# Performance work log

Hardware: AMD Instinct MI355X
Metric: run time of the kernel (lower is better)

The kernel has to match this reference:

```python
import jax, jax.numpy as jnp
import numpy as np

EPS = 1e-16
LOG_2PI = float(np.log(2.0 * np.pi))
DUMMY = -2.0 * float(np.log(10.0))  # dummy component logit / log-prob


def setup_inputs() -> dict:
    key = jax.random.key(0)
    k1, k2, k3, k4, k5 = jax.random.split(key, 5)
    B, N, V, D = 32, 1024, 512, 4
    x = jax.random.normal(k1, (B, N, D), dtype=jnp.float32)
    votes = jax.random.normal(k2, (B, V, D), dtype=jnp.float32)
    # positive stds in [0.1, 1.0)
    scales = jax.random.uniform(k3, (B, V), dtype=jnp.float32) * 0.9 + 0.1
    vote_presence_prob = jax.random.uniform(k4, (B, V), dtype=jnp.float32)
    presence = jax.random.uniform(k5, (B, N), dtype=jnp.float32)
    return {"x": x, "votes": votes, "scales": scales,
            "vote_presence_prob": vote_presence_prob,
            "presence": presence, "n_votes": 16}


def reference(x, votes, scales, vote_presence_prob, presence, n_votes):
    B, N, D = x.shape
    V = votes.shape[1]
    # Broadcast Normal log-prob: x [B,N,1,D] vs votes [B,1,V,D], scale [B,1,V,1]
    sig = scales[:, None, :, None]
    z = (x[:, :, None, :] - votes[:, None, :, :]) / sig
    lp_per_dim = -0.5 * z * z - jnp.log(sig) - 0.5 * LOG_2PI
    vote_log_prob = jnp.sum(lp_per_dim, axis=-1)                       # [B,N,V]
    vote_log_prob = jnp.concatenate(
        [vote_log_prob, jnp.full((B, N, 1), DUMMY, vote_log_prob.dtype)], axis=2)  # [B,N,V+1]

    mixing_logits = jnp.log(vote_presence_prob + EPS)                  # safe_log, [B,V]
    mixing_logits = jnp.concatenate(
        [mixing_logits, jnp.full((B, 1), DUMMY, mixing_logits.dtype)], axis=1)     # [B,V+1]
    mixing_log_prob = jax.nn.log_softmax(mixing_logits, axis=1)        # [B,V+1]

    posterior = mixing_log_prob[:, None, :] + vote_log_prob            # [B,N,V+1]
    mixture_lp_per_comp = jax.scipy.special.logsumexp(posterior, axis=2)  # [B,N]
    mixture_lp_per_comp = mixture_lp_per_comp * presence
    log_prob = jnp.sum(mixture_lp_per_comp)                            # scalar

    winning_vote_idx = jnp.argmax(posterior[:, :, :-1], axis=2)        # [B,N]
    winner = jnp.take_along_axis(votes, winning_vote_idx[:, :, None], axis=1)  # [B,N,D]
    winner_pres = jnp.take_along_axis(vote_presence_prob, winning_vote_idx, axis=1)  # [B,N]
    vote_presence = (mixing_logits[:, :-1] > mixing_logits[:, -1:]).astype(jnp.float32)  # [B,V]
    is_from_capsule = winning_vote_idx // n_votes                      # [B,N]
    posterior_mixing_probs = jax.nn.softmax(posterior, axis=-1)[..., :-1]  # [B,N,V]

    return (log_prob, vote_presence, winner, winner_pres, is_from_capsule,
            mixing_logits, mixing_log_prob, jnp.zeros_like(winner),
            jnp.zeros_like(winner_pres), posterior_mixing_probs)
```

## Files before the change

### kernel.cpp

```cpp
#include <hip/hip_runtime.h>

#define FEPS 1e-16f
#define LOG_2PI 1.8378770664093453f
#define DUMMYV -4.605170185988091f

constexpr int B = 32, N = 1024, V = 512, D = 4;

constexpr long long OFF_LOGPROB    = 0;
constexpr long long OFF_VOTEPRES   = 1;
constexpr long long OFF_WINNER     = OFF_VOTEPRES + (long long)B * V;
constexpr long long OFF_WINNERPRES = OFF_WINNER + (long long)B * N * D;
constexpr long long OFF_ISFROM     = OFF_WINNERPRES + (long long)B * N;
constexpr long long OFF_MLOGITS    = OFF_ISFROM + (long long)B * N;
constexpr long long OFF_MLOGPROB   = OFF_MLOGITS + (long long)B * (V + 1);
constexpr long long OFF_ZW         = OFF_MLOGPROB + (long long)B * (V + 1);
constexpr long long OFF_ZWP        = OFF_ZW + (long long)B * N * D;
constexpr long long OFF_PMP        = OFF_ZWP + (long long)B * N;

__global__ __launch_bounds__(256) void k_fused(const float* __restrict__ x,
                                               const float* __restrict__ votes,
                                               const float* __restrict__ scales,
                                               const float* __restrict__ vpp,
                                               const float* __restrict__ presence,
                                               const int* __restrict__ nv_p,
                                               float* __restrict__ out,
                                               float* __restrict__ ws_partial) {
    __shared__ float4 s_v4[V];
    __shared__ float s_h[V], s_cpre[V], s_lg[V], s_vpp[V];
    __shared__ float s_redm[4], s_reds[4], s_part[4];

    int b = blockIdx.y;
    int t = threadIdx.x;
    int w = t >> 6, lane = t & 63;

    float lgv[2];
    #pragma unroll
    for (int i = 0; i < 2; ++i) {
        int v = t + i * 256;
        float4 vt = reinterpret_cast<const float4*>(votes)[(long long)b * V + v];
        float sv  = scales[(long long)b * V + v];
        float pp  = vpp[(long long)b * V + v];
        float lg  = logf(pp + FEPS);
        float inv = 1.0f / sv;
        s_v4[v]   = vt;
        s_vpp[v]  = pp;
        s_lg[v]   = lg;
        s_h[v]    = 0.5f * inv * inv;
        s_cpre[v] = lg - 4.0f * logf(sv) - 2.0f * LOG_2PI;
        lgv[i] = lg;
    }
    __syncthreads();

    float m = fmaxf(lgv[0], lgv[1]);
    #pragma unroll
    for (int o = 32; o > 0; o >>= 1) m = fmaxf(m, __shfl_xor(m, o));
    if (lane == 0) s_redm[w] = m;
    __syncthreads();
    float M = fmaxf(fmaxf(fmaxf(s_redm[0], s_redm[1]), fmaxf(s_redm[2], s_redm[3])), DUMMYV);
    float s = expf(lgv[0] - M) + expf(lgv[1] - M);
    #pragma unroll
    for (int o = 32; o > 0; o >>= 1) s += __shfl_xor(s, o);
    if (lane == 0) s_reds[w] = s;
    __syncthreads();
    float S = s_reds[0] + s_reds[1] + s_reds[2] + s_reds[3] + expf(DUMMYV - M);
    float lse = M + logf(S);

    float hk[8], c2k[8], hvx[8], hvy[8], hvz[8], hvw[8];
    #pragma unroll
    for (int k = 0; k < 8; ++k) {
        int v = k * 64 + lane;
        float4 vv = s_v4[v];
        float h = s_h[v];
        float c = s_cpre[v] - lse;
        float v2 = vv.x * vv.x + vv.y * vv.y + vv.z * vv.z + vv.w * vv.w;
        hk[k]  = h;
        c2k[k] = c - h * v2;
        hvx[k] = 2.0f * h * vv.x;
        hvy[k] = 2.0f * h * vv.y;
        hvz[k] = 2.0f * h * vv.z;
        hvw[k] = 2.0f * h * vv.w;
    }
    float dummy_post = DUMMYV + (DUMMYV - lse);
    int nv = nv_p[0];
    float acc = 0.f;

    #pragma unroll
    for (int iter = 0; iter < 4; ++iter) {
        int n = blockIdx.x * 16 + iter * 4 + w;
        long long bn = (long long)b * N + n;
        float4 xv = reinterpret_cast<const float4*>(x)[bn];
        float nxx2 = -(xv.x * xv.x + xv.y * xv.y + xv.z * xv.z + xv.w * xv.w);

        float p[8];
        float bv = -1e30f;
        int bi = 0;
        #pragma unroll
        for (int k = 0; k < 8; ++k) {
            float pv = fmaf(hk[k], nxx2, c2k[k]);
            pv = fmaf(hvx[k], xv.x, pv);
            pv = fmaf(hvy[k], xv.y, pv);
            pv = fmaf(hvz[k], xv.z, pv);
            pv = fmaf(hvw[k], xv.w, pv);
            p[k] = pv;
            if (pv > bv) { bv = pv; bi = k * 64 + lane; }
        }
        #pragma unroll
        for (int o = 32; o > 0; o >>= 1) {
            float ov = __shfl_xor(bv, o);
            int   oi = __shfl_xor(bi, o);
            if (ov > bv || (ov == bv && oi < bi)) { bv = ov; bi = oi; }
        }

        float M2 = fmaxf(bv, dummy_post);
        float e[8];
        float lsum = 0.f;
        #pragma unroll
        for (int k = 0; k < 8; ++k) { e[k] = __expf(p[k] - M2); lsum += e[k]; }
        #pragma unroll
        for (int o = 32; o > 0; o >>= 1) lsum += __shfl_xor(lsum, o);
        float total = lsum + __expf(dummy_post - M2);
        float rtot  = 1.0f / total;

        long long base = OFF_PMP + bn * V;
        #pragma unroll
        for (int k = 0; k < 8; ++k)
            out[base + k * 64 + lane] = e[k] * rtot;

        if (lane == 0) {
            acc += (M2 + logf(total)) * presence[bn];
            float4 wv = s_v4[bi];
            out[OFF_WINNER + bn * 4 + 0] = wv.x;
            out[OFF_WINNER + bn * 4 + 1] = wv.y;
            out[OFF_WINNER + bn * 4 + 2] = wv.z;
            out[OFF_WINNER + bn * 4 + 3] = wv.w;
            out[OFF_WINNERPRES + bn]     = s_vpp[bi];
            out[OFF_ISFROM + bn]         = (float)(bi / nv);
        }
        if (lane == 1) {
            out[OFF_ZW + bn * 4 + 0] = 0.f;
            out[OFF_ZW + bn * 4 + 1] = 0.f;
            out[OFF_ZW + bn * 4 + 2] = 0.f;
            out[OFF_ZW + bn * 4 + 3] = 0.f;
            out[OFF_ZWP + bn]        = 0.f;
        }
    }

    if (lane == 0) s_part[w] = acc;
    __syncthreads();
    if (t == 0)
        ws_partial[(long long)b * gridDim.x + blockIdx.x] =
            s_part[0] + s_part[1] + s_part[2] + s_part[3];

    if (blockIdx.x == 0) {
        #pragma unroll
        for (int i = 0; i < 2; ++i) {
            int v = t + i * 256;
            float ml = s_lg[v];
            out[OFF_MLOGITS  + (long long)b * (V + 1) + v] = ml;
            out[OFF_MLOGPROB + (long long)b * (V + 1) + v] = ml - lse;
            out[OFF_VOTEPRES + (long long)b * V + v]       = (ml > DUMMYV) ? 1.0f : 0.0f;
        }
        if (t == 0) {
            out[OFF_MLOGITS  + (long long)b * (V + 1) + V] = DUMMYV;
            out[OFF_MLOGPROB + (long long)b * (V + 1) + V] = DUMMYV - lse;
        }
    }
}

__global__ __launch_bounds__(256) void k_reduce(const float* __restrict__ ws_partial,
                                                float* __restrict__ out, int count) {
    __shared__ float sred[256];
    int t = threadIdx.x;
    float s = 0.f;
    for (int i = t; i < count; i += 256) s += ws_partial[i];
    sred[t] = s;
    __syncthreads();
    for (int o = 128; o > 0; o >>= 1) {
        if (t < o) sred[t] += sred[t + o];
        __syncthreads();
    }
    if (t == 0) out[OFF_LOGPROB] = sred[0];
}

extern "C" void kernel_launch(void* const* d_in, const int* in_sizes, int n_in,
                              void* d_out, int out_size, void* d_ws, size_t ws_size,
                              hipStream_t stream) {
    const float* x        = (const float*)d_in[0];
    const float* votes    = (const float*)d_in[1];
    const float* scales   = (const float*)d_in[2];
    const float* vpp      = (const float*)d_in[3];
    const float* presence = (const float*)d_in[4];
    const int*   nv       = (const int*)d_in[5];
    float* out = (float*)d_out;
    float* ws  = (float*)d_ws;

    dim3 g(N / 16, B);
    k_fused<<<g, 256, 0, stream>>>(x, votes, scales, vpp, presence, nv, out, ws);
    k_reduce<<<1, 256, 0, stream>>>(ws, out, (N / 16) * B);
}
```

Before: 31.88 us.

## Rewrite fused mixture kernel with DPP reductions, packed math, and dummy-relative exp2

Each wave now computes its own per-batch coefficients directly from global memory, so the shared-memory staging and block barriers for the vote tables are gone. Logits are pre-shifted by the dummy posterior and scaled by log2(e), so a raw exp2 replaces the per-row max subtraction and the total becomes sum plus one. Argmax becomes a wave max followed by a min-index search. Wave reductions use DPP row rotates, and the inner product uses packed two-wide float vectors. Each block handles twice as many rows, which halves the number of blocks and partial sums and amortises setup, at the risk of exp2 overflow with no max subtraction.

```diff
diff --git a/kernel.cpp b/kernel.cpp
--- a/kernel.cpp
+++ b/kernel.cpp
@@ -1,140 +1,216 @@
 #include <hip/hip_runtime.h>
+
+typedef float v2f __attribute__((ext_vector_type(2)));
 
 #define FEPS 1e-16f
 #define LOG_2PI 1.8378770664093453f
 #define DUMMYV -4.605170185988091f
-
-constexpr int B = 32, N = 1024, V = 512, D = 4;
+#define LOG2E 1.4426950408889634f
+#define LN2 0.6931471805599453f
+
+constexpr int B = 32, N = 1024, V = 512;
 
 constexpr long long OFF_LOGPROB    = 0;
 constexpr long long OFF_VOTEPRES   = 1;
 constexpr long long OFF_WINNER     = OFF_VOTEPRES + (long long)B * V;
-constexpr long long OFF_WINNERPRES = OFF_WINNER + (long long)B * N * D;
+constexpr long long OFF_WINNERPRES = OFF_WINNER + (long long)B * N * 4;
 constexpr long long OFF_ISFROM     = OFF_WINNERPRES + (long long)B * N;
 constexpr long long OFF_MLOGITS    = OFF_ISFROM + (long long)B * N;
 constexpr long long OFF_MLOGPROB   = OFF_MLOGITS + (long long)B * (V + 1);
 constexpr long long OFF_ZW         = OFF_MLOGPROB + (long long)B * (V + 1);
-constexpr long long OFF_ZWP        = OFF_ZW + (long long)B * N * D;
+constexpr long long OFF_ZWP        = OFF_ZW + (long long)B * N * 4;
 constexpr long long OFF_PMP        = OFF_ZWP + (long long)B * N;
+
+__device__ __forceinline__ float fexp2(float x) {
+#if __has_builtin(__builtin_amdgcn_exp2f)
+    return __builtin_amdgcn_exp2f(x);
+#else
+    return __expf(x * LN2);
+#endif
+}
+__device__ __forceinline__ float frcp(float x) {
+#if __has_builtin(__builtin_amdgcn_rcpf)
+    return __builtin_amdgcn_rcpf(x);
+#else
+    return 1.0f / x;
+#endif
+}
+
+template<int RN> __device__ __forceinline__ float dppRorF(float x) {
+    return __int_as_float(__builtin_amdgcn_update_dpp(
+        0, __float_as_int(x), 0x120 | RN, 0xF, 0xF, false));
+}
+template<int RN> __device__ __forceinline__ int dppRorI(int x) {
+    return __builtin_amdgcn_update_dpp(0, x, 0x120 | RN, 0xF, 0xF, false);
+}
+
+__device__ __forceinline__ float waveMaxF(float m) {
+    m = fmaxf(m, dppRorF<1>(m));
+    m = fmaxf(m, dppRorF<2>(m));
+    m = fmaxf(m, dppRorF<4>(m));
+    m = fmaxf(m, dppRorF<8>(m));
+    m = fmaxf(m, __shfl_xor(m, 16));
+    m = fmaxf(m, __shfl_xor(m, 32));
+    return m;
+}
+__device__ __forceinline__ float waveSumF(float s) {
+    s += dppRorF<1>(s);
+    s += dppRorF<2>(s);
+    s += dppRorF<4>(s);
+    s += dppRorF<8>(s);
+    s += __shfl_xor(s, 16);
+    s += __shfl_xor(s, 32);
+    return s;
+}
+__device__ __forceinline__ int waveMinI(int v) {
+    int o;
+    o = dppRorI<1>(v); v = o < v ? o : v;
+    o = dppRorI<2>(v); v = o < v ? o : v;
+    o = dppRorI<4>(v); v = o < v ? o : v;
+    o = dppRorI<8>(v); v = o < v ? o : v;
+    o = __shfl_xor(v, 16); v = o < v ? o : v;
+    o = __shfl_xor(v, 32); v = o < v ? o : v;
+    return v;
+}
 
 __global__ __launch_bounds__(256) void k_fused(const float* __restrict__ x,
                                                const float* __restrict__ votes,
                                                const float* __restrict__ scales,
                                                const float* __restrict__ vpp,
                                                const float* __restrict__ presence,
-                                               const int* __restrict__ nv_p,
+                                               const int* __restrict__ nvp,
                                                float* __restrict__ out,
-                                               float* __restrict__ ws_partial) {
-    __shared__ float4 s_v4[V];
-    __shared__ float s_h[V], s_cpre[V], s_lg[V], s_vpp[V];
-    __shared__ float s_redm[4], s_reds[4], s_part[4];
-
-    int b = blockIdx.y;
-    int t = threadIdx.x;
-    int w = t >> 6, lane = t & 63;
-
-    float lgv[2];
-    #pragma unroll
-    for (int i = 0; i < 2; ++i) {
-        int v = t + i * 256;
-        float4 vt = reinterpret_cast<const float4*>(votes)[(long long)b * V + v];
-        float sv  = scales[(long long)b * V + v];
-        float pp  = vpp[(long long)b * V + v];
-        float lg  = logf(pp + FEPS);
-        float inv = 1.0f / sv;
-        s_v4[v]   = vt;
-        s_vpp[v]  = pp;
-        s_lg[v]   = lg;
-        s_h[v]    = 0.5f * inv * inv;
-        s_cpre[v] = lg - 4.0f * logf(sv) - 2.0f * LOG_2PI;
-        lgv[i] = lg;
-    }
-    __syncthreads();
-
-    float m = fmaxf(lgv[0], lgv[1]);
-    #pragma unroll
-    for (int o = 32; o > 0; o >>= 1) m = fmaxf(m, __shfl_xor(m, o));
-    if (lane == 0) s_redm[w] = m;
-    __syncthreads();
-    float M = fmaxf(fmaxf(fmaxf(s_redm[0], s_redm[1]), fmaxf(s_redm[2], s_redm[3])), DUMMYV);
-    float s = expf(lgv[0] - M) + expf(lgv[1] - M);
-    #pragma unroll
-    for (int o = 32; o > 0; o >>= 1) s += __shfl_xor(s, o);
-    if (lane == 0) s_reds[w] = s;
-    __syncthreads();
-    float S = s_reds[0] + s_reds[1] + s_reds[2] + s_reds[3] + expf(DUMMYV - M);
-    float lse = M + logf(S);
-
-    float hk[8], c2k[8], hvx[8], hvy[8], hvz[8], hvw[8];
+                                               float* __restrict__ ws) {
+    __shared__ float s_part[4];
+    const int b = blockIdx.y, t = threadIdx.x, w = t >> 6, lane = t & 63;
+    const long long bV = (long long)b * V;
+    const float4* votes4 = reinterpret_cast<const float4*>(votes) + bV;
+
+    float lg[8], lsv[8];
+    float4 vt[8];
     #pragma unroll
     for (int k = 0; k < 8; ++k) {
         int v = k * 64 + lane;
-        float4 vv = s_v4[v];
-        float h = s_h[v];
-        float c = s_cpre[v] - lse;
-        float v2 = vv.x * vv.x + vv.y * vv.y + vv.z * vv.z + vv.w * vv.w;
-        hk[k]  = h;
-        c2k[k] = c - h * v2;
-        hvx[k] = 2.0f * h * vv.x;
-        hvy[k] = 2.0f * h * vv.y;
-        hvz[k] = 2.0f * h * vv.z;
-        hvw[k] = 2.0f * h * vv.w;
-    }
+        vt[k]  = votes4[v];
+        lsv[k] = scales[bV + v];
+        lg[k]  = __logf(vpp[bV + v] + FEPS);
+    }
+
+    float mm = lg[0];
+    #pragma unroll
+    for (int k = 1; k < 8; ++k) mm = fmaxf(mm, lg[k]);
+    float M = fmaxf(waveMaxF(mm), DUMMYV);
+    float ss = 0.f;
+    #pragma unroll
+    for (int k = 0; k < 8; ++k) ss += __expf(lg[k] - M);
+    float S = waveSumF(ss) + __expf(DUMMYV - M);
+    float lse = M + __logf(S);
     float dummy_post = DUMMYV + (DUMMYV - lse);
-    int nv = nv_p[0];
+
+    if (blockIdx.x == 0 && w == 0) {
+        #pragma unroll
+        for (int k = 0; k < 8; ++k) {
+            int v = k * 64 + lane;
+            out[OFF_MLOGITS  + (long long)b * (V + 1) + v] = lg[k];
+            out[OFF_MLOGPROB + (long long)b * (V + 1) + v] = lg[k] - lse;
+            out[OFF_VOTEPRES + bV + v] = (lg[k] > DUMMYV) ? 1.0f : 0.0f;
+        }
+        if (lane == 0) {
+            out[OFF_MLOGITS  + (long long)b * (V + 1) + V] = DUMMYV;
+            out[OFF_MLOGPROB + (long long)b * (V + 1) + V] = DUMMYV - lse;
+        }
+    }
+
+    v2f c2[4], hk[4], hvx[4], hvy[4], hvz[4], hvw[4];
+    #pragma unroll
+    for (int i = 0; i < 4; ++i) {
+        float cc[2], kk[2], ax[2], ay[2], az[2], aw[2];
+        #pragma unroll
+        for (int h = 0; h < 2; ++h) {
+            int k = 2 * i + h;
+            float sv  = lsv[k];
+            float inv = frcp(sv);
+            float hh  = 0.5f * inv * inv;
+            float c   = lg[k] - 4.0f * __logf(sv) - 2.0f * LOG_2PI - lse;
+            float4 vv = vt[k];
+            float v2  = vv.x * vv.x + vv.y * vv.y + vv.z * vv.z + vv.w * vv.w;
+            cc[h] = (c - hh * v2 - dummy_post) * LOG2E;
+            kk[h] = -hh * LOG2E;
+            float g = 2.0f * hh * LOG2E;
+            ax[h] = g * vv.x; ay[h] = g * vv.y; az[h] = g * vv.z; aw[h] = g * vv.w;
+        }
+        c2[i].x = cc[0];  c2[i].y = cc[1];
+        hk[i].x = kk[0];  hk[i].y = kk[1];
+        hvx[i].x = ax[0]; hvx[i].y = ax[1];
+        hvy[i].x = ay[0]; hvy[i].y = ay[1];
+        hvz[i].x = az[0]; hvz[i].y = az[1];
+        hvw[i].x = aw[0]; hvw[i].y = aw[1];
+    }
+
+    const float4* x4 = reinterpret_cast<const float4*>(x) + (long long)b * N;
+    const long long pmpB = OFF_PMP + ((long long)b * N) * V;
+    int nv = nvp[0];
     float acc = 0.f;
 
-    #pragma unroll
-    for (int iter = 0; iter < 4; ++iter) {
-        int n = blockIdx.x * 16 + iter * 4 + w;
+    #pragma unroll 2
+    for (int iter = 0; iter < 8; ++iter) {
+        int n = blockIdx.x * 32 + iter * 4 + w;
         long long bn = (long long)b * N + n;
-        float4 xv = reinterpret_cast<const float4*>(x)[bn];
-        float nxx2 = -(xv.x * xv.x + xv.y * xv.y + xv.z * xv.z + xv.w * xv.w);
-
-        float p[8];
-        float bv = -1e30f;
-        int bi = 0;
-        #pragma unroll
-        for (int k = 0; k < 8; ++k) {
-            float pv = fmaf(hk[k], nxx2, c2k[k]);
-            pv = fmaf(hvx[k], xv.x, pv);
-            pv = fmaf(hvy[k], xv.y, pv);
-            pv = fmaf(hvz[k], xv.z, pv);
-            pv = fmaf(hvw[k], xv.w, pv);
-            p[k] = pv;
-            if (pv > bv) { bv = pv; bi = k * 64 + lane; }
-        }
-        #pragma unroll
-        for (int o = 32; o > 0; o >>= 1) {
-            float ov = __shfl_xor(bv, o);
-            int   oi = __shfl_xor(bi, o);
-            if (ov > bv || (ov == bv && oi < bi)) { bv = ov; bi = oi; }
-        }
-
-        float M2 = fmaxf(bv, dummy_post);
+        float4 xv = x4[n];
+        float px2 = xv.x * xv.x + xv.y * xv.y + xv.z * xv.z + xv.w * xv.w;
+        v2f P2; P2.x = px2;  P2.y = px2;
+        v2f Xx; Xx.x = xv.x; Xx.y = xv.x;
+        v2f Xy; Xy.x = xv.y; Xy.y = xv.y;
+        v2f Xz; Xz.x = xv.z; Xz.y = xv.z;
+        v2f Xw; Xw.x = xv.w; Xw.y = xv.w;
+
+        float p2s[8];
+        #pragma unroll
+        for (int i = 0; i < 4; ++i) {
+            v2f tt = c2[i];
+            tt += hk[i]  * P2;
+            tt += hvx[i] * Xx;
+            tt += hvy[i] * Xy;
+            tt += hvz[i] * Xz;
+            tt += hvw[i] * Xw;
+            p2s[2 * i]     = tt.x;
+            p2s[2 * i + 1] = tt.y;
+        }
+
+        float t1 = fmaxf(fmaxf(p2s[0], p2s[1]), p2s[2]);
+        float t2 = fmaxf(fmaxf(p2s[3], p2s[4]), p2s[5]);
+        float t3 = fmaxf(fmaxf(p2s[6], p2s[7]), t1);
+        float m_in = fmaxf(t2, t3);
+        float Mrow = waveMaxF(m_in);
+
+        int kw = 7;
+        #pragma unroll
+        for (int k = 6; k >= 0; --k) kw = (p2s[k] == Mrow) ? k : kw;
+        int cand = (m_in == Mrow) ? (kw * 64 + lane) : 0x7fffffff;
+        int bi = waveMinI(cand);
+
         float e[8];
-        float lsum = 0.f;
-        #pragma unroll
-        for (int k = 0; k < 8; ++k) { e[k] = __expf(p[k] - M2); lsum += e[k]; }
-        #pragma unroll
-        for (int o = 32; o > 0; o >>= 1) lsum += __shfl_xor(lsum, o);
-        float total = lsum + __expf(dummy_post - M2);
-        float rtot  = 1.0f / total;
-
-        long long base = OFF_PMP + bn * V;
+        float se = 0.f;
+        #pragma unroll
+        for (int k = 0; k < 8; ++k) { e[k] = fexp2(p2s[k]); se += e[k]; }
+        se = waveSumF(se);
+        float total = se + 1.0f;
+        float rt = frcp(total);
+
+        long long pb = pmpB + (long long)n * V;
         #pragma unroll
         for (int k = 0; k < 8; ++k)
-            out[base + k * 64 + lane] = e[k] * rtot;
+            out[pb + k * 64 + lane] = e[k] * rt;
 
         if (lane == 0) {
-            acc += (M2 + logf(total)) * presence[bn];
-            float4 wv = s_v4[bi];
+            acc += (dummy_post + LN2 * __log2f(total)) * presence[bn];
+            float4 wv = votes4[bi];
             out[OFF_WINNER + bn * 4 + 0] = wv.x;
             out[OFF_WINNER + bn * 4 + 1] = wv.y;
             out[OFF_WINNER + bn * 4 + 2] = wv.z;
             out[OFF_WINNER + bn * 4 + 3] = wv.w;
-            out[OFF_WINNERPRES + bn]     = s_vpp[bi];
-            out[OFF_ISFROM + bn]         = (float)(bi / nv);
+            out[OFF_WINNERPRES + bn]     = vpp[bV + bi];
+            out[OFF_ISFROM + bn]         = (float)((nv == 16) ? (bi >> 4) : (bi / nv));
         }
         if (lane == 1) {
             out[OFF_ZW + bn * 4 + 0] = 0.f;
@@ -148,31 +224,16 @@
     if (lane == 0) s_part[w] = acc;
     __syncthreads();
     if (t == 0)
-        ws_partial[(long long)b * gridDim.x + blockIdx.x] =
+        ws[(long long)b * gridDim.x + blockIdx.x] =
             s_part[0] + s_part[1] + s_part[2] + s_part[3];
-
-    if (blockIdx.x == 0) {
-        #pragma unroll
-        for (int i = 0; i < 2; ++i) {
-            int v = t + i * 256;
-            float ml = s_lg[v];
-            out[OFF_MLOGITS  + (long long)b * (V + 1) + v] = ml;
-            out[OFF_MLOGPROB + (long long)b * (V + 1) + v] = ml - lse;
-            out[OFF_VOTEPRES + (long long)b * V + v]       = (ml > DUMMYV) ? 1.0f : 0.0f;
-        }
-        if (t == 0) {
-            out[OFF_MLOGITS  + (long long)b * (V + 1) + V] = DUMMYV;
-            out[OFF_MLOGPROB + (long long)b * (V + 1) + V] = DUMMYV - lse;
-        }
-    }
-}
-
-__global__ __launch_bounds__(256) void k_reduce(const float* __restrict__ ws_partial,
+}
+
+__global__ __launch_bounds__(256) void k_reduce(const float* __restrict__ ws,
                                                 float* __restrict__ out, int count) {
     __shared__ float sred[256];
     int t = threadIdx.x;
     float s = 0.f;
-    for (int i = t; i < count; i += 256) s += ws_partial[i];
+    for (int i = t; i < count; i += 256) s += ws[i];
     sred[t] = s;
     __syncthreads();
     for (int o = 128; o > 0; o >>= 1) {
@@ -194,7 +255,7 @@
     float* out = (float*)d_out;
     float* ws  = (float*)d_ws;
 
-    dim3 g(N / 16, B);
+    dim3 g(N / 32, B);
     k_fused<<<g, 256, 0, stream>>>(x, votes, scales, vpp, presence, nv, out, ws);
-    k_reduce<<<1, 256, 0, stream>>>(ws, out, (N / 16) * B);
-}
+    k_reduce<<<1, 256, 0, stream>>>(ws, out, (N / 32) * B);
+}
```

New measurement: 26.76 us. 1.19x faster.
